# Kernel tuning notes

Hardware: AMD Instinct MI355X
Metric: run time of the kernel (lower is better)

## Reference

```python
import jax, jax.numpy as jnp
import numpy as np

B, T, F, L, E, H, A, V = 64, 32, 512, 196, 512, 512, 512, 10000


def setup_inputs() -> dict:
    key = jax.random.key(0)
    ks = jax.random.split(key, 24)
    s = 0.02
    features = jax.random.normal(ks[0], (B, F, L), dtype=jnp.float32)
    captions = jax.random.randint(ks[1], (B, T), 0, V)
    lengths = jnp.sort(jax.random.randint(ks[2], (B,), 2, T + 1))[::-1]
    lengths = lengths.at[0].set(T)  # ensure max(decode_lengths) == T-1 (static)
    return {
        "features": features,
        "captions": captions,
        "lengths": lengths,
        "W_emb": jax.random.normal(ks[3], (V, E)) * s,
        "W_enc": jax.random.normal(ks[4], (A, F)) * s,
        "b_enc": jnp.zeros((A,)),
        "W_dec": jax.random.normal(ks[5], (A, H)) * s,
        "b_dec": jnp.zeros((A,)),
        "W_full": jax.random.normal(ks[6], (1, A)) * s,
        "b_full": jnp.zeros((1,)),
        "W_fbeta": jax.random.normal(ks[7], (F, H)) * s,
        "b_fbeta": jnp.zeros((F,)),
        "W_ih": jax.random.normal(ks[8], (4 * H, E + F)) * s,
        "W_hh": jax.random.normal(ks[9], (4 * H, H)) * s,
        "b_ih": jnp.zeros((4 * H,)),
        "b_hh": jnp.zeros((4 * H,)),
        "W_out": jax.random.normal(ks[10], (V, H)) * s,
        "b_out": jnp.zeros((V,)),
        "W_init_h": jax.random.normal(ks[11], (H, F)) * s,
        "b_init_h": jnp.zeros((H,)),
        "W_init_c": jax.random.normal(ks[12], (H, F)) * s,
        "b_init_c": jnp.zeros((H,)),
    }


def reference(features, captions, lengths, W_emb, W_enc, b_enc, W_dec, b_dec,
              W_full, b_full, W_fbeta, b_fbeta, W_ih, W_hh, b_ih, b_hh,
              W_out, b_out, W_init_h, b_init_h, W_init_c, b_init_c):
    Bv, Fv, Lv = features.shape
    Tmax = captions.shape[1] - 1  # max(decode_lengths), static (lengths[0]==T)
    feat_r = features.reshape(Bv, -1, Fv)          # [B, L, F] (torch .view semantics)
    en_att = feat_r @ W_enc.T + b_enc              # [B, L, A], step-invariant
    mean_f = features.mean(axis=2)                 # [B, F]
    h0 = mean_f @ W_init_h.T + b_init_h            # [B, H]
    c0 = mean_f @ W_init_c.T + b_init_c
    emb = W_emb[captions]                          # [B, T, E]
    dec_len = lengths - 1                          # [B]

    def step(carry, xs):
        h, c = carry
        emb_t, i = xs
        de = h @ W_dec.T + b_dec                                   # [B, A]
        full = (jnp.tanh(en_att + de[:, None, :]) @ W_full.T)[..., 0] + b_full[0]  # [B, L]
        alpha = jax.nn.softmax(full, axis=1)                       # [B, L]
        z = jnp.einsum('blf,bl->bf', feat_r, alpha)                # [B, F]
        z = z * jax.nn.sigmoid(h @ W_fbeta.T + b_fbeta)
        x = jnp.concatenate([emb_t, z], axis=1)                    # [B, E+F]
        gates = x @ W_ih.T + b_ih + h @ W_hh.T + b_hh              # [B, 4H]
        ig, fg, gg, og = jnp.split(gates, 4, axis=1)
        c_new = jax.nn.sigmoid(fg) * c + jax.nn.sigmoid(ig) * jnp.tanh(gg)
        h_new = jax.nn.sigmoid(og) * jnp.tanh(c_new)
        out = h_new @ W_out.T + b_out                              # [B, V] (dropout: eval)
        active = (dec_len > i)[:, None]                            # ragged mask
        h = jnp.where(active, h_new, h)
        c = jnp.where(active, c_new, c)
        pred = jnp.where(active, out, 0.0)
        alpha_m = jnp.where(active, alpha, 0.0)
        return (h, c), (pred, alpha_m)

    emb_steps = jnp.swapaxes(emb[:, :Tmax, :], 0, 1)               # [Tmax, B, E]
    (_, _), (preds, alphas) = jax.lax.scan(step, (h0, c0), (emb_steps, jnp.arange(Tmax)))
    predictions = jnp.swapaxes(preds, 0, 1)                        # [B, Tmax, V]
    alphas = jnp.swapaxes(alphas, 0, 1)                            # [B, Tmax, L]
    return predictions, alphas
```

## Files before the change

kernel.cpp:

```cpp
#include <hip/hip_runtime.h>


typedef unsigned short ushort_t;
typedef __attribute__((ext_vector_type(8))) short short8;
typedef __attribute__((ext_vector_type(4))) float f32x4;

__device__ __forceinline__ float bf2f(ushort_t u) {
    unsigned x = ((unsigned)u) << 16;
    float f;
    __builtin_memcpy(&f, &x, 4);
    return f;
}
__device__ __forceinline__ ushort_t f2bf(float f) {
    unsigned x;
    __builtin_memcpy(&x, &f, 4);
    unsigned r = (x + 0x7fffu + ((x >> 16) & 1u)) >> 16;
    return (ushort_t)r;
}
__device__ __forceinline__ float sigmoidf_(float x) { return 1.f / (1.f + __expf(-x)); }
__device__ __forceinline__ float tanh_fast(float x) {
    float e = __expf(2.f * x);
    return 1.f - 2.f / (e + 1.f);
}
__device__ __forceinline__ float wred_sum(float v) {
    #pragma unroll
    for (int m = 32; m; m >>= 1) v += __shfl_xor(v, m, 64);
    return v;
}
__device__ __forceinline__ float wred_max(float v) {
    #pragma unroll
    for (int m = 32; m; m >>= 1) v = fmaxf(v, __shfl_xor(v, m, 64));
    return v;
}

__device__ __forceinline__ float aload_f(const float* p) {
    return __hip_atomic_load((float*)p, __ATOMIC_RELAXED, __HIP_MEMORY_SCOPE_AGENT);
}
__device__ __forceinline__ void astore_f(float* p, float v) {
    __hip_atomic_store(p, v, __ATOMIC_RELAXED, __HIP_MEMORY_SCOPE_AGENT);
}
__device__ __forceinline__ unsigned aload_u(const unsigned* p) {
    return __hip_atomic_load((unsigned*)p, __ATOMIC_RELAXED, __HIP_MEMORY_SCOPE_AGENT);
}
__device__ __forceinline__ void astore_u(unsigned* p, unsigned v) {
    __hip_atomic_store(p, v, __ATOMIC_RELAXED, __HIP_MEMORY_SCOPE_AGENT);
}
__device__ __forceinline__ int aload_i(const int* p) {
    return __hip_atomic_load((int*)p, __ATOMIC_RELAXED, __HIP_MEMORY_SCOPE_AGENT);
}

#define KEXP2 2.8853901817779268f

__global__ void detect_kernel(const unsigned* __restrict__ feat_raw, int* __restrict__ flag,
                              int* __restrict__ slots) {
    int lane = threadIdx.x;
    #pragma unroll
    for (int i = 0; i < 4; ++i) slots[lane + i * 64] = 0;
    unsigned u = feat_raw[lane];
    unsigned e = (u >> 7) & 0xffu;
    bool bf_like = (e >= 105 && e <= 133);
    unsigned long long m = __ballot(bf_like);
    if (lane == 0) *flag = (__popcll(m) >= 40) ? 0 : 1;
}

#define NCVT 19
struct CvtArgs {
    const void* src[NCVT];
    void* dst[NCVT];
    int n[NCVT];
};

__global__ __launch_bounds__(256) void convert_kernel(CvtArgs a, const int* __restrict__ flag) {
    const int ai = blockIdx.y;
    const int n = a.n[ai];
    const int base = (blockIdx.x * 256 + threadIdx.x) * 8;
    if (base >= n) return;
    ushort_t* dst = (ushort_t*)a.dst[ai];
    if (*flag) {
        const float* s = (const float*)a.src[ai];
        #pragma unroll
        for (int i = 0; i < 8; ++i) {
            int idx = base + i;
            if (idx < n) dst[idx] = f2bf(s[idx]);
        }
    } else {
        const ushort_t* s = (const ushort_t*)a.src[ai];
        #pragma unroll
        for (int i = 0; i < 8; ++i) {
            int idx = base + i;
            if (idx < n) dst[idx] = s[idx];
        }
    }
}

__global__ __launch_bounds__(256) void embrows_kernel(const void* __restrict__ Wemb,
                                                      const int* __restrict__ captions,
                                                      const int* __restrict__ flag,
                                                      ushort_t* __restrict__ emb_c) {
    const int tb = blockIdx.x;
    const int t = tb >> 6, b = tb & 63;
    const int cap = captions[b * 32 + t];
    const int e0 = threadIdx.x;
    if (*flag) {
        const float* s = (const float*)Wemb + cap * 512;
        emb_c[tb * 512 + e0] = f2bf(s[e0]);
        emb_c[tb * 512 + e0 + 256] = f2bf(s[e0 + 256]);
    } else {
        const ushort_t* s = (const ushort_t*)Wemb + cap * 512;
        emb_c[tb * 512 + e0] = s[e0];
        emb_c[tb * 512 + e0 + 256] = s[e0 + 256];
    }
}

__global__ void prepw2_kernel(const ushort_t* __restrict__ wf, const ushort_t* __restrict__ bfc,
                              float* __restrict__ w2) {
    int tid = threadIdx.x;
    float w = bf2f(wf[tid]);
    w2[tid] = -2.f * w;
    float s = wred_sum(w);
    __shared__ float r8[8];
    if ((tid & 63) == 0) r8[tid >> 6] = s;
    __syncthreads();
    if (tid == 0) {
        float tot = r8[0] + r8[1] + r8[2] + r8[3] + r8[4] + r8[5] + r8[6] + r8[7];
        w2[512] = tot + bf2f(bfc[0]);
    }
}

template <class AROW, class BROW, class EPI>
__device__ __forceinline__ void gemm_tile(AROW arow, BROW brow, EPI epi) {
    __shared__ __align__(16) ushort_t As[64][40];
    __shared__ __align__(16) ushort_t Bs[64][40];
    const int tid = threadIdx.x;
    const int row = tid >> 2, ks = (tid & 3) << 3;
    const int wave = tid >> 6, lane = tid & 63;
    const int quad = lane >> 4, l15 = lane & 15;
    f32x4 acc[4];
    #pragma unroll
    for (int s = 0; s < 4; ++s) acc[s] = (f32x4){0.f, 0.f, 0.f, 0.f};
    const ushort_t* ap = arow(row);
    const ushort_t* bp = brow(row);
    for (int k0 = 0; k0 < 512; k0 += 32) {
        short8 av = {0, 0, 0, 0, 0, 0, 0, 0};
        short8 bv = {0, 0, 0, 0, 0, 0, 0, 0};
        if (ap) av = *(const short8*)(ap + k0 + ks);
        if (bp) bv = *(const short8*)(bp + k0 + ks);
        __syncthreads();
        *(short8*)&As[row][ks] = av;
        *(short8*)&Bs[row][ks] = bv;
        __syncthreads();
        short8 af = *(const short8*)&As[(wave << 4) + l15][quad << 3];
        #pragma unroll
        for (int s = 0; s < 4; ++s) {
            short8 bfr = *(const short8*)&Bs[(s << 4) + l15][quad << 3];
            acc[s] = __builtin_amdgcn_mfma_f32_16x16x32_bf16(af, bfr, acc[s], 0, 0, 0);
        }
    }
    epi((wave << 4) + (quad << 2), l15, acc);
}

__global__ __launch_bounds__(256) void mean_kernel(const ushort_t* __restrict__ features,
                                                   ushort_t* __restrict__ mean_bf) {
    const int b = blockIdx.x;
    const int wave = threadIdx.x >> 6, lane = threadIdx.x & 63;
    const ushort_t* fb = features + b * 512 * 196;
    for (int f = wave; f < 512; f += 4) {
        const ushort_t* r = fb + f * 196;
        float s = bf2f(r[lane]) + bf2f(r[lane + 64]) + bf2f(r[lane + 128]);
        if (lane < 4) s += bf2f(r[lane + 192]);
        s = wred_sum(s);
        if (lane == 0) mean_bf[b * 512 + f] = f2bf(s * (1.f / 196.f));
    }
}

__global__ __launch_bounds__(256) void init_kernel(
    const ushort_t* __restrict__ mean_bf, const ushort_t* __restrict__ Winh,
    const ushort_t* __restrict__ binh, const ushort_t* __restrict__ Winc,
    const ushort_t* __restrict__ binc, ushort_t* __restrict__ h_bf,
    float* __restrict__ cbuf) {
    const int n0 = blockIdx.x << 6;
    gemm_tile(
        [&](int r) { return mean_bf + r * 512; },
        [&](int r) {
            int n = n0 + r;
            return (n < 512) ? (Winh + n * 512) : (Winc + (n - 512) * 512);
        },
        [&](int mb, int l15, const f32x4* acc) {
            #pragma unroll
            for (int s = 0; s < 4; ++s) {
                int n = n0 + (s << 4) + l15;
                #pragma unroll
                for (int r = 0; r < 4; ++r) {
                    int b = mb + r;
                    if (n < 512)
                        h_bf[b * 512 + n] = f2bf(acc[s][r] + bf2f(binh[n]));
                    else
                        cbuf[b * 512 + (n - 512)] = acc[s][r] + bf2f(binc[n - 512]);
                }
            }
        });
}

__global__ __launch_bounds__(256) void enatt_kernel(const ushort_t* __restrict__ feat,
                                                    const ushort_t* __restrict__ Wenc,
                                                    const ushort_t* __restrict__ benc,
                                                    ushort_t* __restrict__ en_att) {
    const int m0 = blockIdx.y << 6, n0 = blockIdx.x << 6;
    gemm_tile(
        [&](int r) { return feat + (m0 + r) * 512; },
        [&](int r) { return Wenc + (n0 + r) * 512; },
        [&](int mb, int l15, const f32x4* acc) {
            #pragma unroll
            for (int s = 0; s < 4; ++s) {
                int n = n0 + (s << 4) + l15;
                float bias = bf2f(benc[n]);
                #pragma unroll
                for (int r = 0; r < 4; ++r) {
                    int m = m0 + mb + r;
                    en_att[m * 512 + n] = f2bf(acc[s][r] + bias);
                }
            }
        });
}

__global__ __launch_bounds__(256) void ec_kernel(const ushort_t* __restrict__ emb_c,
                                                 const ushort_t* __restrict__ Wih,
                                                 const ushort_t* __restrict__ bih,
                                                 const ushort_t* __restrict__ bhh,
                                                 float* __restrict__ ec) {
    const int t = blockIdx.y, n0 = blockIdx.x << 6;
    gemm_tile(
        [&](int r) { return emb_c + (t * 64 + r) * 512; },
        [&](int r) { return Wih + (n0 + r) * 1024; },
        [&](int mb, int l15, const f32x4* acc) {
            #pragma unroll
            for (int s = 0; s < 4; ++s) {
                int j = n0 + (s << 4) + l15;
                float bias = bf2f(bih[j]) + bf2f(bhh[j]);
                #pragma unroll
                for (int r = 0; r < 4; ++r) {
                    int b = mb + r;
                    ec[(t * 64 + b) * 2048 + j] = acc[s][r] + bias;
                }
            }
        });
}

__device__ __forceinline__ void gbar(int* slots, int e) {
    asm volatile("s_waitcnt vmcnt(0)" ::: "memory");
    __syncthreads();
    const int tid = threadIdx.x;
    if (tid == 0)
        __hip_atomic_store(slots + blockIdx.x, e, __ATOMIC_RELAXED,
                           __HIP_MEMORY_SCOPE_AGENT);
    if (tid < 64) {
        for (;;) {
            int a = aload_i(slots + tid);
            int b = aload_i(slots + tid + 64);
            int c = aload_i(slots + tid + 128);
            int d = aload_i(slots + tid + 192);
            if (__all(min(min(a, b), min(c, d)) >= e)) break;
            __builtin_amdgcn_s_sleep(2);
        }
    }
    __syncthreads();
}

struct LoopArgs {
    const ushort_t* W3c;
    const ushort_t* bdec;
    const ushort_t* bfb;
    const ushort_t* en_att;
    const ushort_t* feat;
    const ushort_t* Wih;
    const float* w2;
    const float* ec;
    const int* lengths;
    const int* flag;
    ushort_t* h_bf;
    ushort_t* z_bf;
    ushort_t* H_all;
    float* cbuf;
    float* deK;
    float* fgate;
    float* hh;
    float* fullv;
    void* out_base;
    int* bar;
};

__global__ __launch_bounds__(512, 2) void loop_kernel(LoopArgs A) {
    const int blk = blockIdx.x, tid = threadIdx.x;
    const int wave = tid >> 6, lane = tid & 63;
    const int quad = lane >> 4, l15 = lane & 15;

    __shared__ __align__(16) ushort_t enS[49 * 512];
    __shared__ __align__(16) ushort_t ftS[196 * 128];
    __shared__ __align__(16) ushort_t AsL[16][520];
    __shared__ float smem[2048];
    __shared__ float red8[16];

    const int f32o = *A.flag;
    const int bB = blk >> 2;
    const int qB = blk & 3;
    const int lenB = A.lengths[bB];

    const int mtA = blk & 3;
    const int ntbA = (blk >> 2) << 3;
    const int b0A = mtA << 4;
    const int lenA = A.lengths[b0A + l15];

    const int dtC = blk >> 2;
    const int b0C = (blk & 3) << 4;
    const int lenC = A.lengths[b0C + l15];

    unsigned* h_u32 = (unsigned*)A.h_bf;
    unsigned* z_u32 = (unsigned*)A.z_bf;

    float w2r[8];
    {
        f32x4 w0 = *(const f32x4*)(A.w2 + lane * 8);
        f32x4 w1 = *(const f32x4*)(A.w2 + lane * 8 + 4);
        w2r[0] = w0[0]; w2r[1] = w0[1]; w2r[2] = w0[2]; w2r[3] = w0[3];
        w2r[4] = w1[0]; w2r[5] = w1[1]; w2r[6] = w1[2]; w2r[7] = w1[3];
    }
    const float fullc = A.w2[512];

    {
        const short8* src = (const short8*)(A.en_att + ((size_t)bB * 196 + qB * 49) * 512);
        short8* dst = (short8*)enS;
        for (int i = tid; i < 49 * 64; i += 512) dst[i] = src[i];
        const ushort_t* fsrc = A.feat + (size_t)bB * 100352 + qB * 128;
        short8* fdst = (short8*)ftS;
        for (int i = tid; i < 196 * 16; i += 512) {
            int l = i >> 4, c = i & 15;
            fdst[i] = *(const short8*)(fsrc + l * 512 + c * 8);
        }
    }

    int bt = 0;
    for (int t = 0; t < 31; ++t) {
        if (blk < 96) {
            bool anyact = __any(lenA - 1 > t);
            if (anyact) {
                for (int i = tid; i < 4096; i += 512) {
                    int r = i >> 8, c = i & 255;
                    unsigned v = aload_u(h_u32 + (b0A + r) * 256 + c);
                    *(unsigned*)&AsL[r][c << 1] = v;
                }
                __syncthreads();
                const int nt = ntbA + wave;
                const ushort_t* br = A.W3c + ((nt << 4) + l15) * 512 + (quad << 3);
                const ushort_t* arl = &AsL[l15][quad << 3];
                f32x4 acc = {0.f, 0.f, 0.f, 0.f};
                #pragma unroll
                for (int k0 = 0; k0 < 512; k0 += 32)
                    acc = __builtin_amdgcn_mfma_f32_16x16x32_bf16(
                        *(const short8*)(arl + k0), *(const short8*)(br + k0), acc, 0, 0, 0);
                const int n = (nt << 4) + l15;
                #pragma unroll
                for (int r = 0; r < 4; ++r) {
                    const int b = b0A + (quad << 2) + r;
                    float v = acc[r];
                    if (n < 512)
                        astore_f(A.deK + b * 512 + n, (v + bf2f(A.bdec[n])) * KEXP2);
                    else if (n < 1024)
                        astore_f(A.fgate + b * 512 + (n - 512),
                                 sigmoidf_(v + bf2f(A.bfb[n - 512])));
                    else
                        astore_f(A.hh + b * 2048 + (n - 1024), v);
                }
            }
        }
        ++bt; gbar(A.bar, bt);

        if ((lenB - 1) > t) {
            float dkr[8];
            const float* dk = A.deK + bB * 512 + lane * 8;
            #pragma unroll
            for (int j = 0; j < 8; ++j) dkr[j] = aload_f(dk + j);
            for (int i = wave; i < 49; i += 8) {
                short8 ev = *(const short8*)(enS + i * 512 + lane * 8);
                float acc = 0.f;
                #pragma unroll
                for (int j = 0; j < 8; ++j) {
                    float e2 = __builtin_amdgcn_exp2f(
                        fmaf(bf2f((ushort_t)ev[j]), KEXP2, dkr[j]));
                    acc = fmaf(w2r[j], __builtin_amdgcn_rcpf(e2 + 1.f), acc);
                }
                acc = wred_sum(acc);
                if (lane == 0) astore_f(A.fullv + bB * 196 + qB * 49 + i, acc + fullc);
            }
        }
        ++bt; gbar(A.bar, bt);

        {
            const bool act = (lenB - 1) > t;
            const size_t aoff = 19840000ull + ((size_t)bB * 31 + t) * 196;
            if (!act) {
                if (qB == 0 && tid < 196) {
                    if (f32o) ((float*)A.out_base)[aoff + tid] = 0.f;
                    else ((ushort_t*)A.out_base)[aoff + tid] = 0;
                }
            } else {
                float v = (tid < 196) ? aload_f(A.fullv + bB * 196 + tid) : -1e30f;
                float wm = wred_max(v);
                if (lane == 0) red8[wave] = wm;
                __syncthreads();
                float mx = fmaxf(fmaxf(fmaxf(red8[0], red8[1]), fmaxf(red8[2], red8[3])),
                                 fmaxf(fmaxf(red8[4], red8[5]), fmaxf(red8[6], red8[7])));
                float e = (tid < 196) ? __expf(v - mx) : 0.f;
                float sw = wred_sum(e);
                if (lane == 0) red8[8 + wave] = sw;
                __syncthreads();
                float tot = red8[8] + red8[9] + red8[10] + red8[11] +
                            red8[12] + red8[13] + red8[14] + red8[15];
                float inv = 1.f / tot;
                float a = e * inv;
                if (tid < 196) {
                    smem[tid] = a;
                    if (qB == 0) {
                        if (f32o) ((float*)A.out_base)[aoff + tid] = a;
                        else ((ushort_t*)A.out_base)[aoff + tid] = f2bf(a);
                    }
                }
                __syncthreads();
                const int fl = tid & 127, g = tid >> 7;
                float zacc = 0.f;
                #pragma unroll 4
                for (int l = g; l < 196; l += 4)
                    zacc = fmaf(smem[l], bf2f(ftS[l * 128 + fl]), zacc);
                smem[256 + (g << 7) + fl] = zacc;
                __syncthreads();
                if (tid < 64) {
                    const int f0l = tid << 1;
                    float z0 = smem[256 + f0l] + smem[384 + f0l] +
                               smem[512 + f0l] + smem[640 + f0l];
                    float z1 = smem[257 + f0l] + smem[385 + f0l] +
                               smem[513 + f0l] + smem[641 + f0l];
                    const int f0 = (qB << 7) + f0l;
                    z0 *= aload_f(A.fgate + bB * 512 + f0);
                    z1 *= aload_f(A.fgate + bB * 512 + f0 + 1);
                    unsigned zp = (unsigned)f2bf(z0) | ((unsigned)f2bf(z1) << 16);
                    astore_u(z_u32 + bB * 256 + (f0 >> 1), zp);
                }
            }
        }
        ++bt; gbar(A.bar, bt);

        if (blk < 128) {
            bool anyact = __any(lenC - 1 > t);
            if (anyact) {
                for (int i = tid; i < 4096; i += 512) {
                    int r = i >> 8, c = i & 255;
                    unsigned v = aload_u(z_u32 + (b0C + r) * 256 + c);
                    *(unsigned*)&AsL[r][c << 1] = v;
                }
                __syncthreads();
                const int g = wave & 3, kh = wave >> 2;
                const int j = (g << 9) + (dtC << 4) + l15;
                const ushort_t* br = A.Wih + j * 1024 + 512 + (kh << 8) + (quad << 3);
                const ushort_t* arl = &AsL[l15][(kh << 8) + (quad << 3)];
                f32x4 acc = {0.f, 0.f, 0.f, 0.f};
                #pragma unroll
                for (int k0 = 0; k0 < 256; k0 += 32)
                    acc = __builtin_amdgcn_mfma_f32_16x16x32_bf16(
                        *(const short8*)(arl + k0), *(const short8*)(br + k0), acc, 0, 0, 0);
                #pragma unroll
                for (int r = 0; r < 4; ++r)
                    smem[(wave << 8) + (((quad << 2) + r) << 4) + l15] = acc[r];
                __syncthreads();
                if (tid < 128) {
                    const int bl = tid >> 3, p = tid & 7;
                    const int b = b0C + bl;
                    const int i0 = (bl << 4) + (p << 1);
                    const int dim = (dtC << 4) + (p << 1);
                    const int eb = (t * 64 + b) * 2048, hb = b * 2048;
                    float ig0 = smem[i0] + smem[1024 + i0] +
                                A.ec[eb + dim] + aload_f(A.hh + hb + dim);
                    float ig1 = smem[i0 + 1] + smem[1025 + i0] +
                                A.ec[eb + dim + 1] + aload_f(A.hh + hb + dim + 1);
                    float fg0 = smem[256 + i0] + smem[1280 + i0] +
                                A.ec[eb + 512 + dim] + aload_f(A.hh + hb + 512 + dim);
                    float fg1 = smem[257 + i0] + smem[1281 + i0] +
                                A.ec[eb + 512 + dim + 1] + aload_f(A.hh + hb + 512 + dim + 1);
                    float gg0 = smem[512 + i0] + smem[1536 + i0] +
                                A.ec[eb + 1024 + dim] + aload_f(A.hh + hb + 1024 + dim);
                    float gg1 = smem[513 + i0] + smem[1537 + i0] +
                                A.ec[eb + 1024 + dim + 1] + aload_f(A.hh + hb + 1024 + dim + 1);
                    float og0 = smem[768 + i0] + smem[1792 + i0] +
                                A.ec[eb + 1536 + dim] + aload_f(A.hh + hb + 1536 + dim);
                    float og1 = smem[769 + i0] + smem[1793 + i0] +
                                A.ec[eb + 1536 + dim + 1] + aload_f(A.hh + hb + 1536 + dim + 1);
                    float co0 = A.cbuf[b * 512 + dim];
                    float co1 = A.cbuf[b * 512 + dim + 1];
                    float cn0 = sigmoidf_(fg0) * co0 + sigmoidf_(ig0) * tanh_fast(gg0);
                    float hn0 = sigmoidf_(og0) * tanh_fast(cn0);
                    float cn1 = sigmoidf_(fg1) * co1 + sigmoidf_(ig1) * tanh_fast(gg1);
                    float hn1 = sigmoidf_(og1) * tanh_fast(cn1);
                    unsigned hp = (unsigned)f2bf(hn0) | ((unsigned)f2bf(hn1) << 16);
                    *(unsigned*)&A.H_all[(t * 64 + b) * 512 + dim] = hp;
                    if (A.lengths[b] - 1 > t) {
                        A.cbuf[b * 512 + dim] = cn0;
                        A.cbuf[b * 512 + dim + 1] = cn1;
                        astore_u(h_u32 + b * 256 + (dim >> 1), hp);
                    }
                }
            }
        }
        ++bt; gbar(A.bar, bt);
    }
}

__global__ __launch_bounds__(256) void preds_kernel(
    const ushort_t* __restrict__ H_all, const ushort_t* __restrict__ Wout,
    const ushort_t* __restrict__ bout, const int* __restrict__ lengths,
    const int* __restrict__ flag, void* __restrict__ out_base) {
    const int t = blockIdx.x, n0 = blockIdx.y << 6;
    const int f32o = *flag;
    gemm_tile(
        [&](int r) { return H_all + (t * 64 + r) * 512; },
        [&](int r) -> const ushort_t* {
            int n = n0 + r;
            return (n < 10000) ? (Wout + n * 512) : (const ushort_t*)nullptr;
        },
        [&](int mb, int l15, const f32x4* acc) {
            #pragma unroll
            for (int s = 0; s < 4; ++s) {
                int n = n0 + (s << 4) + l15;
                if (n >= 10000) continue;
                float bias = bf2f(bout[n]);
                #pragma unroll
                for (int r = 0; r < 4; ++r) {
                    int b = mb + r;
                    bool act = lengths[b] > t + 1;
                    float val = act ? (acc[s][r] + bias) : 0.f;
                    size_t off = (size_t)b * 310000 + t * 10000 + n;
                    if (f32o) ((float*)out_base)[off] = val;
                    else ((ushort_t*)out_base)[off] = act ? f2bf(val) : (ushort_t)0;
                }
            }
        });
}

extern "C" void kernel_launch(void* const* d_in, const int* in_sizes, int n_in,
                              void* d_out, int out_size, void* d_ws, size_t ws_size,
                              hipStream_t stream) {
    const void* features = d_in[0];
    const int* captions = (const int*)d_in[1];
    const int* lengths = (const int*)d_in[2];
    const void* W_emb = d_in[3];

    char* ws = (char*)d_ws;
    size_t o = 0;
    auto alloc = [&](size_t bytes) {
        size_t r = o;
        o += (bytes + 255) & ~(size_t)255;
        return r;
    };
    ushort_t* feat_c  = (ushort_t*)(ws + alloc(6422528ull * 2));
    ushort_t* Wenc_c  = (ushort_t*)(ws + alloc(262144ull * 2));
    ushort_t* benc_c  = (ushort_t*)(ws + alloc(512 * 2));
    ushort_t* W3c     = (ushort_t*)(ws + alloc(3072ull * 512 * 2));
    ushort_t* bdec_c  = (ushort_t*)(ws + alloc(512 * 2));
    ushort_t* wfull_c = (ushort_t*)(ws + alloc(512 * 2));
    ushort_t* bfull_c = (ushort_t*)(ws + alloc(2));
    ushort_t* bfb_c   = (ushort_t*)(ws + alloc(512 * 2));
    ushort_t* Wih_c   = (ushort_t*)(ws + alloc(2097152ull * 2));
    ushort_t* bih_c   = (ushort_t*)(ws + alloc(2048 * 2));
    ushort_t* bhh_c   = (ushort_t*)(ws + alloc(2048 * 2));
    ushort_t* Wout_c  = (ushort_t*)(ws + alloc(5120000ull * 2));
    ushort_t* bout_c  = (ushort_t*)(ws + alloc(10000 * 2));
    ushort_t* Winh_c  = (ushort_t*)(ws + alloc(262144ull * 2));
    ushort_t* binh_c  = (ushort_t*)(ws + alloc(512 * 2));
    ushort_t* Winc_c  = (ushort_t*)(ws + alloc(262144ull * 2));
    ushort_t* binc_c  = (ushort_t*)(ws + alloc(512 * 2));
    ushort_t* emb_c   = (ushort_t*)(ws + alloc(1984ull * 512 * 2));
    ushort_t* en_att  = (ushort_t*)(ws + alloc(12544ull * 512 * 2));
    float*    ec      = (float*)(ws + alloc(1984ull * 2048 * 4));
    ushort_t* H_all   = (ushort_t*)(ws + alloc(1984ull * 512 * 2));
    ushort_t* h_bf    = (ushort_t*)(ws + alloc(64 * 512 * 2));
    float*    cbuf    = (float*)(ws + alloc(64 * 512 * 4));
    float*    deK     = (float*)(ws + alloc(64 * 512 * 4));
    float*    fgate   = (float*)(ws + alloc(64 * 512 * 4));
    float*    hh      = (float*)(ws + alloc(64ull * 2048 * 4));
    ushort_t* z_bf    = (ushort_t*)(ws + alloc(64 * 512 * 2));
    ushort_t* mean_bf = (ushort_t*)(ws + alloc(64 * 512 * 2));
    float*    fullv   = (float*)(ws + alloc(64 * 196 * 4));
    float*    w2buf   = (float*)(ws + alloc(513 * 4));
    int*      flag    = (int*)(ws + alloc(256));
    int*      bar     = (int*)(ws + alloc(256 * 4));

    detect_kernel<<<1, 64, 0, stream>>>((const unsigned*)features, flag, bar);

    CvtArgs ca;
    const void* srcs[NCVT] = {features, d_in[4], d_in[5], d_in[6], d_in[7], d_in[8],
                              d_in[9], d_in[10], d_in[11], d_in[12], d_in[13], d_in[14],
                              d_in[15], d_in[16], d_in[17], d_in[18], d_in[19], d_in[20],
                              d_in[21]};
    void* dsts[NCVT] = {feat_c, Wenc_c, benc_c, W3c , bdec_c, wfull_c, bfull_c,
                        W3c + 262144 , bfb_c, Wih_c, W3c + 524288 ,
                        bih_c, bhh_c, Wout_c, bout_c, Winh_c, binh_c, Winc_c, binc_c};
    int ns[NCVT] = {6422528, 262144, 512, 262144, 512, 512, 1, 262144, 512,
                    2097152, 1048576, 2048, 2048, 5120000, 10000, 262144, 512,
                    262144, 512};
    for (int i = 0; i < NCVT; ++i) {
        ca.src[i] = srcs[i];
        ca.dst[i] = dsts[i];
        ca.n[i] = ns[i];
    }
    convert_kernel<<<dim3(3136, NCVT), 256, 0, stream>>>(ca, flag);
    embrows_kernel<<<1984, 256, 0, stream>>>(W_emb, captions, flag, emb_c);
    prepw2_kernel<<<1, 512, 0, stream>>>(wfull_c, bfull_c, w2buf);

    mean_kernel<<<64, 256, 0, stream>>>(feat_c, mean_bf);
    init_kernel<<<16, 256, 0, stream>>>(mean_bf, Winh_c, binh_c, Winc_c, binc_c,
                                        h_bf, cbuf);
    enatt_kernel<<<dim3(8, 196), 256, 0, stream>>>(feat_c, Wenc_c, benc_c, en_att);
    ec_kernel<<<dim3(32, 31), 256, 0, stream>>>(emb_c, Wih_c, bih_c, bhh_c, ec);

    LoopArgs la;
    la.W3c = W3c; la.bdec = bdec_c; la.bfb = bfb_c;
    la.en_att = en_att; la.feat = feat_c; la.Wih = Wih_c;
    la.w2 = w2buf; la.ec = ec; la.lengths = lengths; la.flag = flag;
    la.h_bf = h_bf; la.z_bf = z_bf; la.H_all = H_all;
    la.cbuf = cbuf; la.deK = deK; la.fgate = fgate; la.hh = hh;
    la.fullv = fullv; la.out_base = d_out; la.bar = bar;
    loop_kernel<<<256, 512, 0, stream>>>(la);

    preds_kernel<<<dim3(31, 157), 256, 0, stream>>>(H_all, Wout_c, bout_c, lengths,
                                                    flag, d_out);
}
```

Baseline: 1.431 ms.

## Shrink persistent loop grid and merge attention score and softmax phases per batch

The persistent recurrent kernel now runs 128 blocks instead of 256. Each of 64 blocks handles one batch row's full attention: scores, softmax and the context vector are computed together, streaming en_att and features from global memory rather than staging quarter slices in LDS. This drops one grid barrier per timestep and the fullv global round trip. The barrier polls fewer slots and sleeps less, and the LSTM-cell phase prefetches its ec and hh operands before the z GEMM. In exchange each attention block does four times the work and rereads larger inputs from global memory or cache every step, and fewer CUs are active.

```diff
diff --git a/kernel.cpp b/kernel.cpp
--- a/kernel.cpp
+++ b/kernel.cpp
@@ -257,10 +257,8 @@
         for (;;) {
             int a = aload_i(slots + tid);
             int b = aload_i(slots + tid + 64);
-            int c = aload_i(slots + tid + 128);
-            int d = aload_i(slots + tid + 192);
-            if (__all(min(min(a, b), min(c, d)) >= e)) break;
-            __builtin_amdgcn_s_sleep(2);
+            if (__all(min(a, b) >= e)) break;
+            __builtin_amdgcn_s_sleep(1);
         }
     }
     __syncthreads();
@@ -284,7 +282,6 @@
     float* deK;
     float* fgate;
     float* hh;
-    float* fullv;
     void* out_base;
     int* bar;
 };
@@ -294,21 +291,20 @@
     const int wave = tid >> 6, lane = tid & 63;
     const int quad = lane >> 4, l15 = lane & 15;
 
-    __shared__ __align__(16) ushort_t enS[49 * 512];
-    __shared__ __align__(16) ushort_t ftS[196 * 128];
     __shared__ __align__(16) ushort_t AsL[16][520];
     __shared__ float smem[2048];
+    __shared__ float deS[512];
+    __shared__ float fullS[200];
     __shared__ float red8[16];
 
     const int f32o = *A.flag;
-    const int bB = blk >> 2;
-    const int qB = blk & 3;
-    const int lenB = A.lengths[bB];
 
     const int mtA = blk & 3;
     const int ntbA = (blk >> 2) << 3;
     const int b0A = mtA << 4;
     const int lenA = A.lengths[b0A + l15];
+
+    const int lenBb = A.lengths[blk & 63];
 
     const int dtC = blk >> 2;
     const int b0C = (blk & 3) << 4;
@@ -325,18 +321,6 @@
         w2r[4] = w1[0]; w2r[5] = w1[1]; w2r[6] = w1[2]; w2r[7] = w1[3];
     }
     const float fullc = A.w2[512];
-
-    {
-        const short8* src = (const short8*)(A.en_att + ((size_t)bB * 196 + qB * 49) * 512);
-        short8* dst = (short8*)enS;
-        for (int i = tid; i < 49 * 64; i += 512) dst[i] = src[i];
-        const ushort_t* fsrc = A.feat + (size_t)bB * 100352 + qB * 128;
-        short8* fdst = (short8*)ftS;
-        for (int i = tid; i < 196 * 16; i += 512) {
-            int l = i >> 4, c = i & 15;
-            fdst[i] = *(const short8*)(fsrc + l * 512 + c * 8);
-        }
-    }
 
     int bt = 0;
     for (int t = 0; t < 31; ++t) {
@@ -374,36 +358,37 @@
         }
         ++bt; gbar(A.bar, bt);
 
-        if ((lenB - 1) > t) {
-            float dkr[8];
-            const float* dk = A.deK + bB * 512 + lane * 8;
-            #pragma unroll
-            for (int j = 0; j < 8; ++j) dkr[j] = aload_f(dk + j);
-            for (int i = wave; i < 49; i += 8) {
-                short8 ev = *(const short8*)(enS + i * 512 + lane * 8);
-                float acc = 0.f;
-                #pragma unroll
-                for (int j = 0; j < 8; ++j) {
-                    float e2 = __builtin_amdgcn_exp2f(
-                        fmaf(bf2f((ushort_t)ev[j]), KEXP2, dkr[j]));
-                    acc = fmaf(w2r[j], __builtin_amdgcn_rcpf(e2 + 1.f), acc);
-                }
-                acc = wred_sum(acc);
-                if (lane == 0) astore_f(A.fullv + bB * 196 + qB * 49 + i, acc + fullc);
-            }
-        }
-        ++bt; gbar(A.bar, bt);
-
-        {
-            const bool act = (lenB - 1) > t;
-            const size_t aoff = 19840000ull + ((size_t)bB * 31 + t) * 196;
+        if (blk < 64) {
+            const int b = blk;
+            const bool act = (lenBb - 1) > t;
+            const size_t aoff = 19840000ull + ((size_t)b * 31 + t) * 196;
             if (!act) {
-                if (qB == 0 && tid < 196) {
+                if (tid < 196) {
                     if (f32o) ((float*)A.out_base)[aoff + tid] = 0.f;
                     else ((ushort_t*)A.out_base)[aoff + tid] = 0;
                 }
             } else {
-                float v = (tid < 196) ? aload_f(A.fullv + bB * 196 + tid) : -1e30f;
+                float fgv = aload_f(A.fgate + b * 512 + tid);
+                deS[tid] = aload_f(A.deK + b * 512 + tid);
+                __syncthreads();
+                float dkr[8];
+                #pragma unroll
+                for (int j = 0; j < 8; ++j) dkr[j] = deS[lane * 8 + j];
+                const ushort_t* enb = A.en_att + (size_t)b * 100352;
+                for (int l = wave; l < 196; l += 8) {
+                    short8 ev = *(const short8*)(enb + l * 512 + lane * 8);
+                    float acc = 0.f;
+                    #pragma unroll
+                    for (int j = 0; j < 8; ++j) {
+                        float e2 = __builtin_amdgcn_exp2f(
+                            fmaf(bf2f((ushort_t)ev[j]), KEXP2, dkr[j]));
+                        acc = fmaf(w2r[j], __builtin_amdgcn_rcpf(e2 + 1.f), acc);
+                    }
+                    acc = wred_sum(acc);
+                    if (lane == 0) fullS[l] = acc + fullc;
+                }
+                __syncthreads();
+                float v = (tid < 196) ? fullS[tid] : -1e30f;
                 float wm = wred_max(v);
                 if (lane == 0) red8[wave] = wm;
                 __syncthreads();
@@ -418,39 +403,52 @@
                 float inv = 1.f / tot;
                 float a = e * inv;
                 if (tid < 196) {
-                    smem[tid] = a;
-                    if (qB == 0) {
-                        if (f32o) ((float*)A.out_base)[aoff + tid] = a;
-                        else ((ushort_t*)A.out_base)[aoff + tid] = f2bf(a);
-                    }
-                }
-                __syncthreads();
-                const int fl = tid & 127, g = tid >> 7;
+                    fullS[tid] = a;
+                    if (f32o) ((float*)A.out_base)[aoff + tid] = a;
+                    else ((ushort_t*)A.out_base)[aoff + tid] = f2bf(a);
+                }
+                __syncthreads();
                 float zacc = 0.f;
+                const ushort_t* fb = A.feat + (size_t)b * 100352 + tid;
                 #pragma unroll 4
-                for (int l = g; l < 196; l += 4)
-                    zacc = fmaf(smem[l], bf2f(ftS[l * 128 + fl]), zacc);
-                smem[256 + (g << 7) + fl] = zacc;
-                __syncthreads();
-                if (tid < 64) {
-                    const int f0l = tid << 1;
-                    float z0 = smem[256 + f0l] + smem[384 + f0l] +
-                               smem[512 + f0l] + smem[640 + f0l];
-                    float z1 = smem[257 + f0l] + smem[385 + f0l] +
-                               smem[513 + f0l] + smem[641 + f0l];
-                    const int f0 = (qB << 7) + f0l;
-                    z0 *= aload_f(A.fgate + bB * 512 + f0);
-                    z1 *= aload_f(A.fgate + bB * 512 + f0 + 1);
-                    unsigned zp = (unsigned)f2bf(z0) | ((unsigned)f2bf(z1) << 16);
-                    astore_u(z_u32 + bB * 256 + (f0 >> 1), zp);
+                for (int l = 0; l < 196; ++l)
+                    zacc = fmaf(fullS[l], bf2f(fb[l * 512]), zacc);
+                zacc *= fgv;
+                smem[tid] = zacc;
+                __syncthreads();
+                if (tid < 256) {
+                    unsigned zp = (unsigned)f2bf(smem[tid * 2]) |
+                                  ((unsigned)f2bf(smem[tid * 2 + 1]) << 16);
+                    astore_u(z_u32 + b * 256 + tid, zp);
                 }
             }
         }
         ++bt; gbar(A.bar, bt);
 
-        if (blk < 128) {
+        {
             bool anyact = __any(lenC - 1 > t);
             if (anyact) {
+                float pe[8], ph[8];
+                #pragma unroll
+                for (int k = 0; k < 8; ++k) { pe[k] = 0.f; ph[k] = 0.f; }
+                if (tid < 128) {
+                    const int bl = tid >> 3, p = tid & 7;
+                    const int bE = b0C + bl;
+                    const int dimE = (dtC << 4) + (p << 1);
+                    const int eb = (t * 64 + bE) * 2048, hb = bE * 2048;
+                    pe[0] = A.ec[eb + dimE];         pe[1] = A.ec[eb + dimE + 1];
+                    pe[2] = A.ec[eb + 512 + dimE];   pe[3] = A.ec[eb + 512 + dimE + 1];
+                    pe[4] = A.ec[eb + 1024 + dimE];  pe[5] = A.ec[eb + 1024 + dimE + 1];
+                    pe[6] = A.ec[eb + 1536 + dimE];  pe[7] = A.ec[eb + 1536 + dimE + 1];
+                    ph[0] = aload_f(A.hh + hb + dimE);
+                    ph[1] = aload_f(A.hh + hb + dimE + 1);
+                    ph[2] = aload_f(A.hh + hb + 512 + dimE);
+                    ph[3] = aload_f(A.hh + hb + 512 + dimE + 1);
+                    ph[4] = aload_f(A.hh + hb + 1024 + dimE);
+                    ph[5] = aload_f(A.hh + hb + 1024 + dimE + 1);
+                    ph[6] = aload_f(A.hh + hb + 1536 + dimE);
+                    ph[7] = aload_f(A.hh + hb + 1536 + dimE + 1);
+                }
                 for (int i = tid; i < 4096; i += 512) {
                     int r = i >> 8, c = i & 255;
                     unsigned v = aload_u(z_u32 + (b0C + r) * 256 + c);
@@ -475,23 +473,14 @@
                     const int b = b0C + bl;
                     const int i0 = (bl << 4) + (p << 1);
                     const int dim = (dtC << 4) + (p << 1);
-                    const int eb = (t * 64 + b) * 2048, hb = b * 2048;
-                    float ig0 = smem[i0] + smem[1024 + i0] +
-                                A.ec[eb + dim] + aload_f(A.hh + hb + dim);
-                    float ig1 = smem[i0 + 1] + smem[1025 + i0] +
-                                A.ec[eb + dim + 1] + aload_f(A.hh + hb + dim + 1);
-                    float fg0 = smem[256 + i0] + smem[1280 + i0] +
-                                A.ec[eb + 512 + dim] + aload_f(A.hh + hb + 512 + dim);
-                    float fg1 = smem[257 + i0] + smem[1281 + i0] +
-                                A.ec[eb + 512 + dim + 1] + aload_f(A.hh + hb + 512 + dim + 1);
-                    float gg0 = smem[512 + i0] + smem[1536 + i0] +
-                                A.ec[eb + 1024 + dim] + aload_f(A.hh + hb + 1024 + dim);
-                    float gg1 = smem[513 + i0] + smem[1537 + i0] +
-                                A.ec[eb + 1024 + dim + 1] + aload_f(A.hh + hb + 1024 + dim + 1);
-                    float og0 = smem[768 + i0] + smem[1792 + i0] +
-                                A.ec[eb + 1536 + dim] + aload_f(A.hh + hb + 1536 + dim);
-                    float og1 = smem[769 + i0] + smem[1793 + i0] +
-                                A.ec[eb + 1536 + dim + 1] + aload_f(A.hh + hb + 1536 + dim + 1);
+                    float ig0 = smem[i0] + smem[1024 + i0] + pe[0] + ph[0];
+                    float ig1 = smem[i0 + 1] + smem[1025 + i0] + pe[1] + ph[1];
+                    float fg0 = smem[256 + i0] + smem[1280 + i0] + pe[2] + ph[2];
+                    float fg1 = smem[257 + i0] + smem[1281 + i0] + pe[3] + ph[3];
+                    float gg0 = smem[512 + i0] + smem[1536 + i0] + pe[4] + ph[4];
+                    float gg1 = smem[513 + i0] + smem[1537 + i0] + pe[5] + ph[5];
+                    float og0 = smem[768 + i0] + smem[1792 + i0] + pe[6] + ph[6];
+                    float og1 = smem[769 + i0] + smem[1793 + i0] + pe[7] + ph[7];
                     float co0 = A.cbuf[b * 512 + dim];
                     float co1 = A.cbuf[b * 512 + dim + 1];
                     float cn0 = sigmoidf_(fg0) * co0 + sigmoidf_(ig0) * tanh_fast(gg0);
@@ -586,7 +575,6 @@
     float*    hh      = (float*)(ws + alloc(64ull * 2048 * 4));
     ushort_t* z_bf    = (ushort_t*)(ws + alloc(64 * 512 * 2));
     ushort_t* mean_bf = (ushort_t*)(ws + alloc(64 * 512 * 2));
-    float*    fullv   = (float*)(ws + alloc(64 * 196 * 4));
     float*    w2buf   = (float*)(ws + alloc(513 * 4));
     int*      flag    = (int*)(ws + alloc(256));
     int*      bar     = (int*)(ws + alloc(256 * 4));
@@ -625,8 +613,8 @@
     la.w2 = w2buf; la.ec = ec; la.lengths = lengths; la.flag = flag;
     la.h_bf = h_bf; la.z_bf = z_bf; la.H_all = H_all;
     la.cbuf = cbuf; la.deK = deK; la.fgate = fgate; la.hh = hh;
-    la.fullv = fullv; la.out_base = d_out; la.bar = bar;
-    loop_kernel<<<256, 512, 0, stream>>>(la);
+    la.out_base = d_out; la.bar = bar;
+    loop_kernel<<<128, 512, 0, stream>>>(la);
 
     preds_kernel<<<dim3(31, 157), 256, 0, stream>>>(H_all, Wout_c, bout_c, lengths,
                                                     flag, d_out);
```

After: 1.842 ms. 1.29x slower.
